# Kernel tuning notes

Measured on AMD Instinct MI355X. Metric: run time of the kernel, lower is better.

## Reference

```python
import jax, jax.numpy as jnp
import numpy as np
from jax import lax

DIM = 384
HEADS = 8
PROMPTDIM = 192
EPS = 1e-12  # torch F.normalize eps


def conv1x1(x, w):
    # x: [b,c,h,w], w: [out,c]
    return jnp.einsum('bchw,oc->bohw', x, w)


def dwconv3x3(x, w):
    # depthwise 3x3, SAME padding; w: [C,1,3,3]
    return lax.conv_general_dilated(
        x, w, window_strides=(1, 1), padding='SAME',
        feature_group_count=x.shape[1],
        dimension_numbers=('NCHW', 'OIHW', 'NCHW'))


def setup_inputs() -> dict:
    key = jax.random.key(0)
    ks = jax.random.split(key, 8)
    b, h, w = 8, 128, 128
    s = 0.05
    return {
        'x': jax.random.normal(ks[0], (b, DIM, h, w), jnp.float32),
        'de': jax.random.normal(ks[1], (b, PROMPTDIM, h, w), jnp.float32),
        'w_qv': jax.random.normal(ks[2], (2 * DIM, DIM), jnp.float32) * s,
        'w_qv_dw': jax.random.normal(ks[3], (2 * DIM, 1, 3, 3), jnp.float32) * s,
        'w_k': jax.random.normal(ks[4], (DIM, PROMPTDIM), jnp.float32) * s,
        'w_k_dw': jax.random.normal(ks[5], (DIM, 1, 3, 3), jnp.float32) * s,
        'w_proj': jax.random.normal(ks[6], (DIM, DIM), jnp.float32) * s,
        'temperature': jnp.ones((HEADS, 1, 1), jnp.float32),
    }


def reference(x, de, w_qv, w_qv_dw, w_k, w_k_dw, w_proj, temperature):
    b, c, h, w = x.shape
    head_c = c // HEADS
    qv = dwconv3x3(conv1x1(x, w_qv), w_qv_dw)          # [b,2c,h,w]
    q, v = qv[:, :c], qv[:, c:]
    k = dwconv3x3(conv1x1(de, w_k), w_k_dw)            # [b,c,h,w]

    def to_heads(t):
        return t.reshape(b, HEADS, head_c, h * w)       # [b,head,c,hw]

    q, k, v = to_heads(q), to_heads(k), to_heads(v)
    # L2-normalize over hw (torch F.normalize: x / max(||x||, eps))
    q = q / jnp.maximum(jnp.linalg.norm(q, axis=-1, keepdims=True), EPS)
    k = k / jnp.maximum(jnp.linalg.norm(k, axis=-1, keepdims=True), EPS)
    attn = jnp.einsum('bhcs,bhds->bhcd', q, k) * temperature  # [b,head,c,c]
    attn = jax.nn.softmax(attn, axis=-1)
    out = jnp.einsum('bhcd,bhds->bhcs', attn, v)        # [b,head,c,hw]
    out = out.reshape(b, c, h, w)
    return conv1x1(out, w_proj)
```

## Files before the change

kernel.cpp:

```cpp
#include <hip/hip_runtime.h>

#define SPATIAL 16384
#define BATCH 8
#define CDIM 384
#define QVDIM 768
#define PDIM 192
#define NHEADS 8
#define HC 48

typedef __attribute__((ext_vector_type(8))) short short8;
typedef __attribute__((ext_vector_type(4))) float f32x4;
typedef __attribute__((ext_vector_type(4))) int i32x4;

__device__ __forceinline__ unsigned short f2bf(float f) {
  union { float f; unsigned u; } v; v.f = f;
  unsigned r = v.u + 0x7fffu + ((v.u >> 16) & 1u);
  return (unsigned short)(r >> 16);
}
__device__ __forceinline__ float bf2f(unsigned short h) {
  union { unsigned u; float f; } v; v.u = ((unsigned)h) << 16;
  return v.f;
}

__device__ __forceinline__ void gload16(const unsigned short* g, unsigned short* lds) {
  __builtin_amdgcn_global_load_lds(
      (const __attribute__((address_space(1))) void*)g,
      (__attribute__((address_space(3))) void*)lds,
      16, 0, 0);
}


__device__ __forceinline__ void w2bf_body(int bid, const float* __restrict__ in,
                                          unsigned short* __restrict__ out, int n) {
  int i = bid * 256 + threadIdx.x;
  if (i < n) out[i] = f2bf(in[i]);
}

__device__ __forceinline__ void transpose_body(int bid, const float* __restrict__ in,
                                               unsigned short* __restrict__ out, int C,
                                               float (*tile)[65]) {
  int st = bid % (SPATIAL / 64); bid /= (SPATIAL / 64);
  int ct = bid % (C / 64); int b = bid / (C / 64);
  int t = threadIdx.x;
  const float* ip = in + ((size_t)b * C + (size_t)ct * 64) * SPATIAL + (size_t)st * 64;
  int fx = t & 15, fy = t >> 4;
#pragma unroll
  for (int i = 0; i < 4; i++) {
    int r = fy + i * 16;
    f32x4 v = *(const f32x4*)(ip + (size_t)r * SPATIAL + fx * 4);
    tile[r][fx * 4 + 0] = v[0];
    tile[r][fx * 4 + 1] = v[1];
    tile[r][fx * 4 + 2] = v[2];
    tile[r][fx * 4 + 3] = v[3];
  }
  __syncthreads();
  unsigned short* op = out + ((size_t)b * SPATIAL + (size_t)st * 64) * C + (size_t)ct * 64;
  int cg = t & 7, sr = t >> 3;
#pragma unroll
  for (int i = 0; i < 2; i++) {
    int s = sr + i * 32;
    short8 o;
#pragma unroll
    for (int j = 0; j < 8; j++) o[j] = (short)f2bf(tile[cg * 8 + j][s]);
    *(short8*)(op + (size_t)s * C + cg * 8) = o;
  }
}

template<int BM, bool OUT_BF16>
__device__ __forceinline__ void gemm_body(int lbid, int nwg,
    const unsigned short* __restrict__ A, const unsigned short* __restrict__ B,
    void* __restrict__ Cv, int M, int K, long strideA, unsigned short* lds)
{
  constexpr int MFR = BM / 32;
  constexpr int ARD = BM / 64;
  constexpr int SL  = ARD + 4;
  constexpr int ASZ = BM * 64;
  constexpr int BUF = ASZ + 256 * 64;

  int bid = (lbid & 7) * (nwg >> 3) + (lbid >> 3);
  int mt = M / BM;
  int mb = bid % mt; bid /= mt;
  int nb = bid & 63; int b = bid >> 6;

  const unsigned short* Ab = A + (size_t)b * strideA + (size_t)mb * BM * K;
  const unsigned short* Bb = B + ((size_t)b * SPATIAL + (size_t)nb * 256) * K;

  int t = threadIdx.x;
  int lane = t & 63;
  int w = t >> 6;
  int wm = (w >> 2) * (BM / 2), wn = (w & 3) * 64;
  int lr = lane & 15, lg = lane >> 4;

  f32x4 acc[MFR][4];
#pragma unroll
  for (int i = 0; i < MFR; i++)
#pragma unroll
    for (int j = 0; j < 4; j++)
      acc[i][j] = (f32x4){0.f, 0.f, 0.f, 0.f};

  int arow = t >> 3;
  int aslot = (t & 7) ^ (arow & 7);
  const unsigned short* gA0 = Ab + (size_t)arow * K + aslot * 8;
  const unsigned short* gB0 = Bb + (size_t)arow * K + aslot * 8;

  auto STAGE = [&](int kt, int q) {
    int k0 = kt * 64;
    unsigned short* base = &lds[q * BUF];
#pragma unroll
    for (int r = 0; r < ARD; ++r)
      gload16(gA0 + (size_t)r * 64 * K + k0, base + r * 4096 + w * 512);
#pragma unroll
    for (int r = 0; r < 4; ++r)
      gload16(gB0 + (size_t)r * 64 * K + k0, base + ASZ + r * 4096 + w * 512);
  };

  int nt = K >> 6;
  STAGE(0, 0);
  STAGE(1, 1);

  int colr0 = ((0 * 4 + lg) ^ (lr & 7)) * 8;
  int colr1 = ((1 * 4 + lg) ^ (lr & 7)) * 8;

  for (int j = 0; j < nt; ++j) {
    if (j + 1 < nt) { asm volatile("s_waitcnt vmcnt(%0)" :: "n"(SL) : "memory"); }
    else            { asm volatile("s_waitcnt vmcnt(0)" ::: "memory"); }
    __builtin_amdgcn_s_barrier();
    __builtin_amdgcn_sched_barrier(0);

    unsigned short* cb = &lds[(j & 1) * BUF];

    {
      short8 af[MFR], bfv[4];
#pragma unroll
      for (int mi = 0; mi < MFR; ++mi)
        af[mi] = *(const short8*)(&cb[(wm + mi * 16 + lr) * 64 + colr0]);
#pragma unroll
      for (int ni = 0; ni < 4; ++ni)
        bfv[ni] = *(const short8*)(&cb[ASZ + (wn + ni * 16 + lr) * 64 + colr0]);
      __builtin_amdgcn_s_setprio(1);
#pragma unroll
      for (int mi = 0; mi < MFR; ++mi)
#pragma unroll
        for (int ni = 0; ni < 4; ++ni)
          acc[mi][ni] = __builtin_amdgcn_mfma_f32_16x16x32_bf16(af[mi], bfv[ni], acc[mi][ni], 0, 0, 0);
      __builtin_amdgcn_s_setprio(0);
    }
    __builtin_amdgcn_sched_barrier(0);
    {
      short8 af[MFR], bfv[4];
#pragma unroll
      for (int mi = 0; mi < MFR; ++mi)
        af[mi] = *(const short8*)(&cb[(wm + mi * 16 + lr) * 64 + colr1]);
#pragma unroll
      for (int ni = 0; ni < 4; ++ni)
        bfv[ni] = *(const short8*)(&cb[ASZ + (wn + ni * 16 + lr) * 64 + colr1]);
      __builtin_amdgcn_s_setprio(1);
#pragma unroll
      for (int mi = 0; mi < MFR; ++mi)
#pragma unroll
        for (int ni = 0; ni < 4; ++ni)
          acc[mi][ni] = __builtin_amdgcn_mfma_f32_16x16x32_bf16(af[mi], bfv[ni], acc[mi][ni], 0, 0, 0);
      __builtin_amdgcn_s_setprio(0);
    }
    __builtin_amdgcn_sched_barrier(0);
    __builtin_amdgcn_s_barrier();
    if (j + 2 < nt) STAGE(j + 2, j & 1);
  }

  size_t rbase = (size_t)mb * BM + wm + lg * 4;
  size_t cbase = (size_t)nb * 256 + wn + lr;
  if (OUT_BF16) {
    unsigned short* C = (unsigned short*)Cv + (size_t)b * M * SPATIAL;
#pragma unroll
    for (int mi = 0; mi < MFR; ++mi)
#pragma unroll
      for (int ni = 0; ni < 4; ++ni) {
        size_t r = rbase + mi * 16;
        size_t c = cbase + ni * 16;
#pragma unroll
        for (int jj = 0; jj < 4; ++jj)
          C[(r + jj) * SPATIAL + c] = f2bf(acc[mi][ni][jj]);
      }
  } else {
    float* C = (float*)Cv + (size_t)b * M * SPATIAL;
#pragma unroll
    for (int mi = 0; mi < MFR; ++mi)
#pragma unroll
      for (int ni = 0; ni < 4; ++ni) {
        size_t r = rbase + mi * 16;
        size_t c = cbase + ni * 16;
#pragma unroll
        for (int jj = 0; jj < 4; ++jj)
          C[(r + jj) * SPATIAL + c] = acc[mi][ni][jj];
      }
  }
}

template<bool NORM>
__device__ __forceinline__ void dwconv_body(int bid, const unsigned short* __restrict__ in,
    const float* __restrict__ wdw, unsigned short* __restrict__ out,
    float* __restrict__ norm2, int C, int in_cstride, int chan_off)
{
  int yt = bid & 7; bid >>= 3;
  int c = bid % C; int b = bid / C;
  const unsigned short* ip = in + ((size_t)b * in_cstride + chan_off + c) * SPATIAL;
  const float* wp = wdw + (size_t)(chan_off + c) * 9;
  float wr[9];
#pragma unroll
  for (int i = 0; i < 9; i++) wr[i] = wp[i];

  int t = threadIdx.x;
  int l = t & 63;
  int g = t & 15;
  int ty = t >> 4, xs = g * 8;
  int y = yt * 16 + ty;

  float acc[8];
#pragma unroll
  for (int j = 0; j < 8; j++) acc[j] = 0.f;

  auto row = [&](int yy, float wa, float wb, float wc) {
    if ((unsigned)yy >= 128u) return;
    const unsigned short* rp = ip + yy * 128 + xs;
    short8 cv = *(const short8*)rp;
    float cf[8];
#pragma unroll
    for (int j = 0; j < 8; j++) cf[j] = bf2f((unsigned short)cv[j]);
    float lf = __shfl(cf[7], (l - 1) & 63, 64);
    float rt = __shfl(cf[0], (l + 1) & 63, 64);
    if (g == 0)  lf = 0.f;
    if (g == 15) rt = 0.f;
    acc[0] += wa * lf + wb * cf[0] + wc * cf[1];
#pragma unroll
    for (int j = 1; j < 7; j++) acc[j] += wa * cf[j - 1] + wb * cf[j] + wc * cf[j + 1];
    acc[7] += wa * cf[6] + wb * cf[7] + wc * rt;
  };
  row(y - 1, wr[0], wr[1], wr[2]);
  row(y,     wr[3], wr[4], wr[5]);
  row(y + 1, wr[6], wr[7], wr[8]);

  short8 o;
  float sq = 0.f;
#pragma unroll
  for (int j = 0; j < 8; j++) {
    o[j] = (short)f2bf(acc[j]);
    if (NORM) { float v = bf2f((unsigned short)o[j]); sq += v * v; }
  }
  *(short8*)(out + ((size_t)b * C + c) * SPATIAL + y * 128 + xs) = o;

  if (NORM) {
#pragma unroll
    for (int off = 32; off > 0; off >>= 1) sq += __shfl_down(sq, off, 64);
    __shared__ float red[4];
    if ((t & 63) == 0) red[t >> 6] = sq;
    __syncthreads();
    if (t == 0)
      atomicAdd(&norm2[(size_t)b * C + c], red[0] + red[1] + red[2] + red[3]);
  }
}

__device__ __forceinline__ void dwt_body(int bid, const unsigned short* __restrict__ qv,
    const float* __restrict__ wdw, unsigned short* __restrict__ vT)
{
  __shared__ float tile[128][17];
  int y = bid & 127; bid >>= 7;
  int ct = bid % 24; int b = bid / 24;
  int t = threadIdx.x;
  int l = t & 63;
  int g = t & 15;
  int ci = t >> 4, xs = g * 8;
  int c = CDIM + ct * 16 + ci;
  const unsigned short* ip = qv + ((size_t)b * QVDIM + c) * SPATIAL;
  const float* wp = wdw + (size_t)c * 9;
  float wr[9];
#pragma unroll
  for (int i = 0; i < 9; i++) wr[i] = wp[i];

  float acc[8];
#pragma unroll
  for (int j = 0; j < 8; j++) acc[j] = 0.f;

  auto row = [&](int yy, float wa, float wb, float wc) {
    if ((unsigned)yy >= 128u) return;
    const unsigned short* rp = ip + yy * 128 + xs;
    short8 cv = *(const short8*)rp;
    float cf[8];
#pragma unroll
    for (int j = 0; j < 8; j++) cf[j] = bf2f((unsigned short)cv[j]);
    float lf = __shfl(cf[7], (l - 1) & 63, 64);
    float rt = __shfl(cf[0], (l + 1) & 63, 64);
    if (g == 0)  lf = 0.f;
    if (g == 15) rt = 0.f;
    acc[0] += wa * lf + wb * cf[0] + wc * cf[1];
#pragma unroll
    for (int j = 1; j < 7; j++) acc[j] += wa * cf[j - 1] + wb * cf[j] + wc * cf[j + 1];
    acc[7] += wa * cf[6] + wb * cf[7] + wc * rt;
  };
  row(y - 1, wr[0], wr[1], wr[2]);
  row(y,     wr[3], wr[4], wr[5]);
  row(y + 1, wr[6], wr[7], wr[8]);

#pragma unroll
  for (int j = 0; j < 8; j++) tile[xs + j][ci] = acc[j];
  __syncthreads();

  int xw = t >> 1, cg = t & 1;
  short8 o;
#pragma unroll
  for (int j = 0; j < 8; j++) o[j] = (short)f2bf(tile[xw][cg * 8 + j]);
  *(short8*)(vT + ((size_t)b * SPATIAL + (size_t)y * 128 + xw) * CDIM + ct * 16 + cg * 8) = o;
}


#define PREP_N1 ((QVDIM * CDIM) / 256)
#define PREP_N2 ((CDIM * PDIM) / 256)
#define PREP_N3 (BATCH * (CDIM / 64) * (SPATIAL / 64))
#define PREP_N4 (BATCH * (PDIM / 64) * (SPATIAL / 64))
__global__ __launch_bounds__(256)
void k_prep(const float* __restrict__ w_qv, unsigned short* __restrict__ wqvb,
            const float* __restrict__ w_k, unsigned short* __restrict__ wkb,
            const float* __restrict__ x, unsigned short* __restrict__ xT,
            const float* __restrict__ de, unsigned short* __restrict__ deT)
{
  __shared__ float tile[64][65];
  int bid = blockIdx.x;
  if (bid < PREP_N1)                      w2bf_body(bid, w_qv, wqvb, QVDIM * CDIM);
  else if (bid < PREP_N1 + PREP_N2)       w2bf_body(bid - PREP_N1, w_k, wkb, CDIM * PDIM);
  else if (bid < PREP_N1 + PREP_N2 + PREP_N3)
    transpose_body(bid - PREP_N1 - PREP_N2, x, xT, CDIM, tile);
  else
    transpose_body(bid - PREP_N1 - PREP_N2 - PREP_N3, de, deT, PDIM, tile);
}

#define G1_N  (BATCH * (QVDIM / 256) * (SPATIAL / 256))
#define G1B_N (BATCH * (CDIM / 128) * (SPATIAL / 256))
__global__ __launch_bounds__(512, 2)
void k_gemms(const unsigned short* __restrict__ A1, const unsigned short* __restrict__ B1,
             void* __restrict__ C1,
             const unsigned short* __restrict__ A2, const unsigned short* __restrict__ B2,
             void* __restrict__ C2)
{
  __shared__ unsigned short lds[2 * (256 * 64 + 256 * 64)];
  int bid = blockIdx.x;
  if (bid < G1_N)
    gemm_body<256, true>(bid, G1_N, A1, B1, C1, QVDIM, CDIM, 0L, lds);
  else
    gemm_body<128, true>(bid - G1_N, G1B_N, A2, B2, C2, CDIM, PDIM, 0L, lds);
}

#define DW_NQ (BATCH * CDIM * 8)
#define DW_NT (BATCH * 24 * 128)
#define DW_NK (BATCH * CDIM * 8)
__global__ __launch_bounds__(256)
void k_dw(const unsigned short* __restrict__ qv, const unsigned short* __restrict__ kpre,
          const float* __restrict__ w_qvdw, const float* __restrict__ w_kdw,
          unsigned short* __restrict__ qdw, unsigned short* __restrict__ kdw,
          unsigned short* __restrict__ vT,
          float* __restrict__ n2q, float* __restrict__ n2k)
{
  int bid = blockIdx.x;
  if (bid < DW_NQ)
    dwconv_body<true>(bid, qv, w_qvdw, qdw, n2q, CDIM, QVDIM, 0);
  else if (bid < DW_NQ + DW_NT)
    dwt_body(bid - DW_NQ, qv, w_qvdw, vT);
  else
    dwconv_body<true>(bid - DW_NQ - DW_NT, kpre, w_kdw, kdw, n2k, CDIM, CDIM, 0);
}

__global__ __launch_bounds__(512, 2)
void k_gemm2(const unsigned short* __restrict__ A, const unsigned short* __restrict__ B,
             void* __restrict__ Cv)
{
  __shared__ unsigned short lds[2 * (128 * 64 + 256 * 64)];
  gemm_body<128, false>(blockIdx.x, gridDim.x, A, B, Cv, CDIM, CDIM, (long)(CDIM * CDIM), lds);
}

__global__ __launch_bounds__(256)
void k_logits(const unsigned short* __restrict__ qd, const unsigned short* __restrict__ kd,
              float* __restrict__ raw)
{
  int bid = blockIdx.x;
  int sp = bid & 15; bid >>= 4;
  int h = bid & 7; int b = bid >> 3;
  int lane = threadIdx.x & 63, wv = threadIdx.x >> 6;
  int lr = lane & 15, lg = lane >> 4;
  const unsigned short* qp = qd + ((size_t)b * CDIM + h * HC) * SPATIAL;
  const unsigned short* kp = kd + ((size_t)b * CDIM + h * HC) * SPATIAL;
  int s0 = sp * 1024 + wv * 256;
  f32x4 acc[3][3];
#pragma unroll
  for (int i = 0; i < 3; i++)
#pragma unroll
    for (int j = 0; j < 3; j++)
      acc[i][j] = (f32x4){0.f, 0.f, 0.f, 0.f};
  for (int ks = 0; ks < 256; ks += 32) {
    int off = s0 + ks + lg * 8;
    short8 qf[3], kf[3];
#pragma unroll
    for (int i = 0; i < 3; i++) {
      qf[i] = *(const short8*)(qp + (size_t)(i * 16 + lr) * SPATIAL + off);
      kf[i] = *(const short8*)(kp + (size_t)(i * 16 + lr) * SPATIAL + off);
    }
#pragma unroll
    for (int ci = 0; ci < 3; ci++)
#pragma unroll
      for (int di = 0; di < 3; di++)
        acc[ci][di] = __builtin_amdgcn_mfma_f32_16x16x32_bf16(qf[ci], kf[di], acc[ci][di], 0, 0, 0);
  }
  float* rp = raw + ((size_t)(b * NHEADS + h)) * HC * HC;
#pragma unroll
  for (int ci = 0; ci < 3; ci++)
#pragma unroll
    for (int di = 0; di < 3; di++)
#pragma unroll
      for (int j = 0; j < 4; j++)
        atomicAdd(&rp[(ci * 16 + lg * 4 + j) * HC + di * 16 + lr], acc[ci][di][j]);
}

__global__ void k_softmax(const float* __restrict__ raw, const float* __restrict__ n2q,
                          const float* __restrict__ n2k, const float* __restrict__ temp,
                          float* __restrict__ attn)
{
  int h = blockIdx.x & 7, b = blockIdx.x >> 3;
  int c = threadIdx.x;
  if (c >= HC) return;
  float tp = temp[h];
  float qn = fmaxf(sqrtf(n2q[b * CDIM + h * HC + c]), 1e-12f);
  const float* rp = raw + ((size_t)(b * NHEADS + h) * HC + c) * HC;
  float vals[HC];
  float mx = -1e30f;
#pragma unroll
  for (int d = 0; d < HC; d++) {
    float kn = fmaxf(sqrtf(n2k[b * CDIM + h * HC + d]), 1e-12f);
    float v = rp[d] * tp / (qn * kn);
    vals[d] = v;
    mx = fmaxf(mx, v);
  }
  float sum = 0.f;
#pragma unroll
  for (int d = 0; d < HC; d++) { vals[d] = expf(vals[d] - mx); sum += vals[d]; }
  float inv = 1.f / sum;
  float* ap = attn + ((size_t)(b * NHEADS + h) * HC + c) * HC;
#pragma unroll
  for (int d = 0; d < HC; d++) ap[d] = vals[d] * inv;
}

__global__ void k_mbuild(const float* __restrict__ attn, const float* __restrict__ wproj,
                         unsigned short* __restrict__ Mb)
{
  int o = blockIdx.x % CDIM, b = blockIdx.x / CDIM;
  int j = threadIdx.x;
  int h = j / HC, d = j % HC;
  const float* wp = wproj + (size_t)o * CDIM + h * HC;
  const float* ap = attn + (size_t)(b * NHEADS + h) * HC * HC + d;
  float s = 0.f;
#pragma unroll
  for (int cp = 0; cp < HC; cp++) s += wp[cp] * ap[cp * HC];
  Mb[((size_t)b * CDIM + o) * CDIM + j] = f2bf(s);
}

static const size_t OFF_QV   = 0;
static const size_t OFF_KDW  = 0;
static const size_t OFF_XT   = 201326592;
static const size_t OFF_QDW  = 201326592;
static const size_t OFF_DET  = 301989888;
static const size_t OFF_VT   = 301989888;
static const size_t OFF_KPRE = 402653184;
static const size_t OFF_WQVB = 503316480;
static const size_t OFF_WKB  = 503906304;
static const size_t OFF_N2Q  = 504053760;
static const size_t OFF_N2K  = 504066048;
static const size_t OFF_RAW  = 504078336;
static const size_t OFF_ATTN = 504668160;
static const size_t OFF_MB   = 505257984;

extern "C" void kernel_launch(void* const* d_in, const int* in_sizes, int n_in,
                              void* d_out, int out_size, void* d_ws, size_t ws_size,
                              hipStream_t stream) {
  const float* x      = (const float*)d_in[0];
  const float* de     = (const float*)d_in[1];
  const float* w_qv   = (const float*)d_in[2];
  const float* w_qvdw = (const float*)d_in[3];
  const float* w_k    = (const float*)d_in[4];
  const float* w_kdw  = (const float*)d_in[5];
  const float* w_proj = (const float*)d_in[6];
  const float* temp   = (const float*)d_in[7];

  char* ws = (char*)d_ws;
  unsigned short* qv    = (unsigned short*)(ws + OFF_QV);
  unsigned short* kdw   = (unsigned short*)(ws + OFF_KDW);
  unsigned short* xT    = (unsigned short*)(ws + OFF_XT);
  unsigned short* qdw   = (unsigned short*)(ws + OFF_QDW);
  unsigned short* deT   = (unsigned short*)(ws + OFF_DET);
  unsigned short* vT    = (unsigned short*)(ws + OFF_VT);
  unsigned short* kpre  = (unsigned short*)(ws + OFF_KPRE);
  unsigned short* wqvb  = (unsigned short*)(ws + OFF_WQVB);
  unsigned short* wkb   = (unsigned short*)(ws + OFF_WKB);
  float* n2q  = (float*)(ws + OFF_N2Q);
  float* n2k  = (float*)(ws + OFF_N2K);
  float* raw  = (float*)(ws + OFF_RAW);
  float* attn = (float*)(ws + OFF_ATTN);
  unsigned short* Mb = (unsigned short*)(ws + OFF_MB);

  hipMemsetAsync(ws + OFF_N2Q, 0, 12288 + 12288 + 589824, stream);

  k_prep<<<dim3(PREP_N1 + PREP_N2 + PREP_N3 + PREP_N4), dim3(256), 0, stream>>>(
      w_qv, wqvb, w_k, wkb, x, xT, de, deT);

  k_gemms<<<dim3(G1_N + G1B_N), dim3(512), 0, stream>>>(
      wqvb, xT, (void*)qv, wkb, deT, (void*)kpre);

  k_dw<<<dim3(DW_NQ + DW_NT + DW_NK), dim3(256), 0, stream>>>(
      qv, kpre, w_qvdw, w_kdw, qdw, kdw, vT, n2q, n2k);

  k_logits<<<dim3(BATCH * NHEADS * 16), dim3(256), 0, stream>>>(qdw, kdw, raw);
  k_softmax<<<dim3(BATCH * NHEADS), dim3(64), 0, stream>>>(raw, n2q, n2k, temp, attn);
  k_mbuild<<<dim3(BATCH * CDIM), dim3(CDIM), 0, stream>>>(attn, w_proj, Mb);

  k_gemm2<<<dim3(BATCH * (CDIM / 128) * (SPATIAL / 256)), dim3(512), 0, stream>>>(
      Mb, vT, d_out);
}
```

Baseline: 579.9 us.

## Process eight rows per thread in depthwise convs with rolling row reuse

Each thread now produces eight consecutive output rows of the 3x3 depthwise conv and keeps a rolling three-row register window, so each input row is loaded once per thread rather than three times. The grid shrinks eightfold accordingly. Because each block now covers a whole channel, the norm reduction writes the per-channel sum directly instead of using an atomicAdd. The cost is fewer, longer-running blocks, more registers per thread, and two barriers per row in the transposing V path.

After: 548.1 us. -5.5%, faster.

```diff
diff --git a/kernel.cpp b/kernel.cpp
--- a/kernel.cpp
+++ b/kernel.cpp
@@ -201,7 +201,6 @@
     const float* __restrict__ wdw, unsigned short* __restrict__ out,
     float* __restrict__ norm2, int C, int in_cstride, int chan_off)
 {
-  int yt = bid & 7; bid >>= 3;
   int c = bid % C; int b = bid / C;
   const unsigned short* ip = in + ((size_t)b * in_cstride + chan_off + c) * SPATIAL;
   const float* wp = wdw + (size_t)(chan_off + c) * 9;
@@ -210,52 +209,64 @@
   for (int i = 0; i < 9; i++) wr[i] = wp[i];
 
   int t = threadIdx.x;
-  int l = t & 63;
-  int g = t & 15;
-  int ty = t >> 4, xs = g * 8;
-  int y = yt * 16 + ty;
-
-  float acc[8];
-#pragma unroll
-  for (int j = 0; j < 8; j++) acc[j] = 0.f;
-
-  auto row = [&](int yy, float wa, float wb, float wc) {
-    if ((unsigned)yy >= 128u) return;
-    const unsigned short* rp = ip + yy * 128 + xs;
-    short8 cv = *(const short8*)rp;
-    float cf[8];
-#pragma unroll
-    for (int j = 0; j < 8; j++) cf[j] = bf2f((unsigned short)cv[j]);
-    float lf = __shfl(cf[7], (l - 1) & 63, 64);
-    float rt = __shfl(cf[0], (l + 1) & 63, 64);
-    if (g == 0)  lf = 0.f;
-    if (g == 15) rt = 0.f;
-    acc[0] += wa * lf + wb * cf[0] + wc * cf[1];
-#pragma unroll
-    for (int j = 1; j < 7; j++) acc[j] += wa * cf[j - 1] + wb * cf[j] + wc * cf[j + 1];
-    acc[7] += wa * cf[6] + wb * cf[7] + wc * rt;
+  int l = t & 63, g = t & 15;
+  int y0 = (t >> 4) * 8;
+  int xs = g * 8;
+  unsigned short* op = out + ((size_t)b * C + c) * SPATIAL + y0 * 128 + xs;
+
+  float rv[3][8], rl[3], rr[3];
+  auto loadrow = [&](int yy, int s) {
+    if ((unsigned)yy < 128u) {
+      short8 cv = *(const short8*)(ip + yy * 128 + xs);
+#pragma unroll
+      for (int j = 0; j < 8; j++) rv[s][j] = bf2f((unsigned short)cv[j]);
+    } else {
+#pragma unroll
+      for (int j = 0; j < 8; j++) rv[s][j] = 0.f;
+    }
+    float lf = __shfl(rv[s][7], (l - 1) & 63, 64);
+    float rt = __shfl(rv[s][0], (l + 1) & 63, 64);
+    rl[s] = (g == 0) ? 0.f : lf;
+    rr[s] = (g == 15) ? 0.f : rt;
   };
-  row(y - 1, wr[0], wr[1], wr[2]);
-  row(y,     wr[3], wr[4], wr[5]);
-  row(y + 1, wr[6], wr[7], wr[8]);
-
-  short8 o;
+
+  loadrow(y0 - 1, 0);
+  loadrow(y0, 1);
+
   float sq = 0.f;
 #pragma unroll
-  for (int j = 0; j < 8; j++) {
-    o[j] = (short)f2bf(acc[j]);
-    if (NORM) { float v = bf2f((unsigned short)o[j]); sq += v * v; }
-  }
-  *(short8*)(out + ((size_t)b * C + c) * SPATIAL + y * 128 + xs) = o;
+  for (int r = 0; r < 8; r++) {
+    const int sp = r % 3, sc = (r + 1) % 3, sn = (r + 2) % 3;
+    loadrow(y0 + r + 1, sn);
+    float acc[8];
+    acc[0] = wr[0]*rl[sp] + wr[1]*rv[sp][0] + wr[2]*rv[sp][1]
+           + wr[3]*rl[sc] + wr[4]*rv[sc][0] + wr[5]*rv[sc][1]
+           + wr[6]*rl[sn] + wr[7]*rv[sn][0] + wr[8]*rv[sn][1];
+#pragma unroll
+    for (int j = 1; j < 7; j++)
+      acc[j] = wr[0]*rv[sp][j-1] + wr[1]*rv[sp][j] + wr[2]*rv[sp][j+1]
+             + wr[3]*rv[sc][j-1] + wr[4]*rv[sc][j] + wr[5]*rv[sc][j+1]
+             + wr[6]*rv[sn][j-1] + wr[7]*rv[sn][j] + wr[8]*rv[sn][j+1];
+    acc[7] = wr[0]*rv[sp][6] + wr[1]*rv[sp][7] + wr[2]*rr[sp]
+           + wr[3]*rv[sc][6] + wr[4]*rv[sc][7] + wr[5]*rr[sc]
+           + wr[6]*rv[sn][6] + wr[7]*rv[sn][7] + wr[8]*rr[sn];
+    short8 o;
+#pragma unroll
+    for (int j = 0; j < 8; j++) {
+      o[j] = (short)f2bf(acc[j]);
+      if (NORM) { float v = bf2f((unsigned short)o[j]); sq += v * v; }
+    }
+    *(short8*)(op + r * 128) = o;
+  }
 
   if (NORM) {
 #pragma unroll
     for (int off = 32; off > 0; off >>= 1) sq += __shfl_down(sq, off, 64);
     __shared__ float red[4];
-    if ((t & 63) == 0) red[t >> 6] = sq;
+    if (l == 0) red[t >> 6] = sq;
     __syncthreads();
     if (t == 0)
-      atomicAdd(&norm2[(size_t)b * C + c], red[0] + red[1] + red[2] + red[3]);
+      norm2[(size_t)b * CDIM + c] = red[0] + red[1] + red[2] + red[3];
   }
 }
 
@@ -263,12 +274,13 @@
     const float* __restrict__ wdw, unsigned short* __restrict__ vT)
 {
   __shared__ float tile[128][17];
-  int y = bid & 127; bid >>= 7;
+  int yt = bid & 15; bid >>= 4;
   int ct = bid % 24; int b = bid / 24;
   int t = threadIdx.x;
-  int l = t & 63;
-  int g = t & 15;
-  int ci = t >> 4, xs = g * 8;
+  int l = t & 63, g = t & 15;
+  int ci = t >> 4;
+  int xs = g * 8;
+  int y0 = yt * 8;
   int c = CDIM + ct * 16 + ci;
   const unsigned short* ip = qv + ((size_t)b * QVDIM + c) * SPATIAL;
   const float* wp = wdw + (size_t)c * 9;
@@ -276,39 +288,51 @@
 #pragma unroll
   for (int i = 0; i < 9; i++) wr[i] = wp[i];
 
-  float acc[8];
-#pragma unroll
-  for (int j = 0; j < 8; j++) acc[j] = 0.f;
-
-  auto row = [&](int yy, float wa, float wb, float wc) {
-    if ((unsigned)yy >= 128u) return;
-    const unsigned short* rp = ip + yy * 128 + xs;
-    short8 cv = *(const short8*)rp;
-    float cf[8];
-#pragma unroll
-    for (int j = 0; j < 8; j++) cf[j] = bf2f((unsigned short)cv[j]);
-    float lf = __shfl(cf[7], (l - 1) & 63, 64);
-    float rt = __shfl(cf[0], (l + 1) & 63, 64);
-    if (g == 0)  lf = 0.f;
-    if (g == 15) rt = 0.f;
-    acc[0] += wa * lf + wb * cf[0] + wc * cf[1];
-#pragma unroll
-    for (int j = 1; j < 7; j++) acc[j] += wa * cf[j - 1] + wb * cf[j] + wc * cf[j + 1];
-    acc[7] += wa * cf[6] + wb * cf[7] + wc * rt;
+  float rv[3][8], rl[3], rr[3];
+  auto loadrow = [&](int yy, int s) {
+    if ((unsigned)yy < 128u) {
+      short8 cv = *(const short8*)(ip + yy * 128 + xs);
+#pragma unroll
+      for (int j = 0; j < 8; j++) rv[s][j] = bf2f((unsigned short)cv[j]);
+    } else {
+#pragma unroll
+      for (int j = 0; j < 8; j++) rv[s][j] = 0.f;
+    }
+    float lf = __shfl(rv[s][7], (l - 1) & 63, 64);
+    float rt = __shfl(rv[s][0], (l + 1) & 63, 64);
+    rl[s] = (g == 0) ? 0.f : lf;
+    rr[s] = (g == 15) ? 0.f : rt;
   };
-  row(y - 1, wr[0], wr[1], wr[2]);
-  row(y,     wr[3], wr[4], wr[5]);
-  row(y + 1, wr[6], wr[7], wr[8]);
-
-#pragma unroll
-  for (int j = 0; j < 8; j++) tile[xs + j][ci] = acc[j];
-  __syncthreads();
+
+  loadrow(y0 - 1, 0);
+  loadrow(y0, 1);
 
   int xw = t >> 1, cg = t & 1;
-  short8 o;
-#pragma unroll
-  for (int j = 0; j < 8; j++) o[j] = (short)f2bf(tile[xw][cg * 8 + j]);
-  *(short8*)(vT + ((size_t)b * SPATIAL + (size_t)y * 128 + xw) * CDIM + ct * 16 + cg * 8) = o;
+#pragma unroll
+  for (int r = 0; r < 8; r++) {
+    const int sp = r % 3, sc = (r + 1) % 3, sn = (r + 2) % 3;
+    loadrow(y0 + r + 1, sn);
+    float acc[8];
+    acc[0] = wr[0]*rl[sp] + wr[1]*rv[sp][0] + wr[2]*rv[sp][1]
+           + wr[3]*rl[sc] + wr[4]*rv[sc][0] + wr[5]*rv[sc][1]
+           + wr[6]*rl[sn] + wr[7]*rv[sn][0] + wr[8]*rv[sn][1];
+#pragma unroll
+    for (int j = 1; j < 7; j++)
+      acc[j] = wr[0]*rv[sp][j-1] + wr[1]*rv[sp][j] + wr[2]*rv[sp][j+1]
+             + wr[3]*rv[sc][j-1] + wr[4]*rv[sc][j] + wr[5]*rv[sc][j+1]
+             + wr[6]*rv[sn][j-1] + wr[7]*rv[sn][j] + wr[8]*rv[sn][j+1];
+    acc[7] = wr[0]*rv[sp][6] + wr[1]*rv[sp][7] + wr[2]*rr[sp]
+           + wr[3]*rv[sc][6] + wr[4]*rv[sc][7] + wr[5]*rr[sc]
+           + wr[6]*rv[sn][6] + wr[7]*rv[sn][7] + wr[8]*rr[sn];
+#pragma unroll
+    for (int j = 0; j < 8; j++) tile[xs + j][ci] = acc[j];
+    __syncthreads();
+    short8 o;
+#pragma unroll
+    for (int j = 0; j < 8; j++) o[j] = (short)f2bf(tile[xw][cg * 8 + j]);
+    *(short8*)(vT + ((size_t)b * SPATIAL + (size_t)(y0 + r) * 128 + xw) * CDIM + ct * 16 + cg * 8) = o;
+    __syncthreads();
+  }
 }
 
 
@@ -348,9 +372,9 @@
     gemm_body<128, true>(bid - G1_N, G1B_N, A2, B2, C2, CDIM, PDIM, 0L, lds);
 }
 
-#define DW_NQ (BATCH * CDIM * 8)
-#define DW_NT (BATCH * 24 * 128)
-#define DW_NK (BATCH * CDIM * 8)
+#define DW_NQ (BATCH * CDIM)
+#define DW_NT (BATCH * 24 * 16)
+#define DW_NK (BATCH * CDIM)
 __global__ __launch_bounds__(256)
 void k_dw(const unsigned short* __restrict__ qv, const unsigned short* __restrict__ kpre,
           const float* __restrict__ w_qvdw, const float* __restrict__ w_kdw,
```
